# Kernel tuning notes

Hardware: AMD Instinct MI355X
Metric: run time of the kernel (lower is better)

Reference implementation:

```python
import jax, jax.numpy as jnp
import numpy as np

H = 4            # num_heads (forced: 128 projection / d_k=32)
DK = 32          # hardcoded d_k
SCALE = 1.0 / np.sqrt(32.0)
EPS = 1e-5       # LayerNorm eps (torch default)


def setup_inputs() -> dict:
    key = jax.random.key(0)
    ks = jax.random.split(key, 8)
    B, L, Dq, Dkv, M = 16, 4096, 512, 512, 512
    def w(k, shape, fan_in):
        return (jax.random.normal(k, shape, jnp.float32) / np.sqrt(fan_in)).astype(jnp.float32)
    return {
        "Q_in":  jax.random.normal(ks[0], (B, L, Dq),  jnp.float32),
        "KV_in": jax.random.normal(ks[1], (B, L, Dkv), jnp.float32),
        "Wq":  w(ks[2], (Dq, 128), Dq),   "bq":  jnp.zeros((128,), jnp.float32),
        "Wk":  w(ks[3], (Dkv, 128), Dkv), "bk":  jnp.zeros((128,), jnp.float32),
        "Wv":  w(ks[4], (Dkv, 128), Dkv), "bv":  jnp.zeros((128,), jnp.float32),
        "Wo":  w(ks[5], (128, M), 128),   "bo":  jnp.zeros((M,), jnp.float32),
        "Wqo": w(ks[6], (128, M), 128),   "bqo": jnp.zeros((M,), jnp.float32),
        "gamma": jnp.ones((M,), jnp.float32),
        "beta":  jnp.zeros((M,), jnp.float32),
    }


def reference(Q_in, KV_in, Wq, bq, Wk, bk, Wv, bv, Wo, bo, Wqo, bqo, gamma, beta):
    B, L, _ = Q_in.shape
    Qm = Q_in @ Wq + bq          # (B, L, 128)
    Km = KV_in @ Wk + bk         # (B, L, 128)
    Vm = KV_in @ Wv + bv         # (B, L, 128)

    def heads(X):
        # view(B, L, H, DK).permute(0, 2, 3, 1) -> (B, H, DK, L)
        return X.reshape(B, L, H, DK).transpose(0, 2, 3, 1)

    Qh, Kh, Vh = heads(Qm), heads(Km), heads(Vm)
    # matmul contracts over the SEQUENCE dim -> feature-feature scores (B,H,DK,DK)
    scores = jnp.einsum('bhdl,bhel->bhde', Qh, Kh) * SCALE
    attn = jax.nn.softmax(scores, axis=-1)          # dropout = identity (eval)
    out_h = jnp.einsum('bhde,bhel->bhdl', attn, Vh)  # (B, H, DK, L)
    out_h = out_h.transpose(0, 3, 1, 2).reshape(B, L, H * DK)  # (B, L, 128)

    out = out_h @ Wo + bo        # (B, L, M)
    Qm_ = Qm @ Wqo + bqo         # (B, L, M)
    x = Qm_ + out
    mu = jnp.mean(x, axis=-1, keepdims=True)
    var = jnp.var(x, axis=-1, keepdims=True)
    y = (x - mu) * jax.lax.rsqrt(var + EPS) * gamma + beta
    return (y, attn)
```

## Files before the change

kernel.cpp:

```cpp
#include <hip/hip_runtime.h>
#include <hip/hip_bf16.h>

typedef __bf16 bf16x8 __attribute__((ext_vector_type(8)));
typedef float  f32x4  __attribute__((ext_vector_type(4)));

#define SCALE_QK 0.17677669529663687f
#define LDSS 40

__device__ __forceinline__ float b2f(ushort u) {
    __hip_bfloat16 h; *reinterpret_cast<ushort*>(&h) = u; return __bfloat162float(h);
}
__device__ __forceinline__ ushort f2b(float f) {
    __hip_bfloat16 h = __float2bfloat16(f); return *reinterpret_cast<ushort*>(&h);
}

__global__ void k_prep(const float* __restrict__ Wq, const float* __restrict__ Wk,
                       const float* __restrict__ Wv, const float* __restrict__ Wqo,
                       const float* __restrict__ Wo,
                       ushort* __restrict__ WqThi, ushort* __restrict__ WqTlo,
                       ushort* __restrict__ WkThi, ushort* __restrict__ WkTlo,
                       ushort* __restrict__ WvT,  ushort* __restrict__ WqoT,
                       ushort* __restrict__ WoB) {
    int idx = blockIdx.x * 256 + threadIdx.x;
    int mat = idx >> 16, i = idx & 65535;
    if (mat == 0) {
        int n = i >> 9, k = i & 511;
        float w = Wq[k * 128 + n];
        ushort hi = f2b(w);
        WqThi[i] = hi; WqTlo[i] = f2b(w - b2f(hi));
    } else if (mat == 1) {
        int n = i >> 9, k = i & 511;
        float w = Wk[k * 128 + n];
        ushort hi = f2b(w);
        WkThi[i] = hi; WkTlo[i] = f2b(w - b2f(hi));
    } else if (mat == 2) {
        int n = i >> 9, k = i & 511;
        WvT[i] = f2b(Wv[k * 128 + n]);
    } else if (mat == 3) {
        int n = i >> 7, k = i & 127;
        WqoT[i] = f2b(Wqo[k * 512 + n]);
    } else if (mat == 4) {
        WoB[i] = f2b(Wo[i]);
    }
}

__global__ __launch_bounds__(256) void k_proj_split(
        const float* __restrict__ A, const ushort* __restrict__ BThi,
        const ushort* __restrict__ BTlo, const float* __restrict__ bias,
        float* __restrict__ outF, ushort* __restrict__ outB) {
    __shared__ __align__(16) ushort AsH[128 * LDSS], AsL[128 * LDSS];
    __shared__ __align__(16) ushort BsH[128 * LDSS], BsL[128 * LDSS];
    const int row0 = blockIdx.x * 128;
    const int tid  = threadIdx.x;
    const int wid  = tid >> 6, lane = tid & 63;
    const int wm = wid >> 1, wn = wid & 1;
    const int quad = lane >> 4, l16 = lane & 15;
    const int sr = tid >> 2;
    const int sc = (tid & 3) * 8;

    f32x4 acc[4][4] = {};

    for (int k0 = 0; k0 < 512; k0 += 32) {
        __syncthreads();
#pragma unroll
        for (int p = 0; p < 2; ++p) {
            int r = sr + p * 64;
            float4 a0 = *(const float4*)&A[(size_t)(row0 + r) * 512 + k0 + sc];
            float4 a1 = *(const float4*)&A[(size_t)(row0 + r) * 512 + k0 + sc + 4];
            float av[8] = {a0.x, a0.y, a0.z, a0.w, a1.x, a1.y, a1.z, a1.w};
            union { uint4 v; ushort u[8]; } H, L;
#pragma unroll
            for (int i = 0; i < 8; ++i) {
                ushort hi = f2b(av[i]);
                H.u[i] = hi;
                L.u[i] = f2b(av[i] - b2f(hi));
            }
            *(uint4*)&AsH[r * LDSS + sc] = H.v;
            *(uint4*)&AsL[r * LDSS + sc] = L.v;
            uint4 bh = *(const uint4*)&BThi[(size_t)r * 512 + k0 + sc];
            uint4 bl = *(const uint4*)&BTlo[(size_t)r * 512 + k0 + sc];
            *(uint4*)&BsH[r * LDSS + sc] = bh;
            *(uint4*)&BsL[r * LDSS + sc] = bl;
        }
        __syncthreads();
        bf16x8 aH[4], aL[4], bH[4], bL[4];
#pragma unroll
        for (int i = 0; i < 4; ++i) {
            int ro = (wm * 64 + i * 16 + l16) * LDSS + quad * 8;
            aH[i] = *reinterpret_cast<const bf16x8*>(&AsH[ro]);
            aL[i] = *reinterpret_cast<const bf16x8*>(&AsL[ro]);
        }
#pragma unroll
        for (int j = 0; j < 4; ++j) {
            int ro = (wn * 64 + j * 16 + l16) * LDSS + quad * 8;
            bH[j] = *reinterpret_cast<const bf16x8*>(&BsH[ro]);
            bL[j] = *reinterpret_cast<const bf16x8*>(&BsL[ro]);
        }
#pragma unroll
        for (int i = 0; i < 4; ++i)
#pragma unroll
            for (int j = 0; j < 4; ++j) {
                acc[i][j] = __builtin_amdgcn_mfma_f32_16x16x32_bf16(aL[i], bH[j], acc[i][j], 0, 0, 0);
                acc[i][j] = __builtin_amdgcn_mfma_f32_16x16x32_bf16(aH[i], bL[j], acc[i][j], 0, 0, 0);
                acc[i][j] = __builtin_amdgcn_mfma_f32_16x16x32_bf16(aH[i], bH[j], acc[i][j], 0, 0, 0);
            }
    }

#pragma unroll
    for (int i = 0; i < 4; ++i)
#pragma unroll
        for (int j = 0; j < 4; ++j) {
            int ncol = wn * 64 + j * 16 + l16;
            float bv = bias[ncol];
#pragma unroll
            for (int r = 0; r < 4; ++r) {
                int mrow = row0 + wm * 64 + i * 16 + quad * 4 + r;
                float v = acc[i][j][r] + bv;
                if (outF) outF[(size_t)mrow * 128 + ncol] = v;
                if (outB) outB[(size_t)mrow * 128 + ncol] = f2b(v);
            }
        }
}

__global__ __launch_bounds__(256) void k_proj_plain(
        const float* __restrict__ A, const ushort* __restrict__ BT,
        const float* __restrict__ bias, ushort* __restrict__ outB) {
    __shared__ __align__(16) ushort As[128 * LDSS];
    __shared__ __align__(16) ushort Bs[128 * LDSS];
    const int row0 = blockIdx.x * 128;
    const int tid  = threadIdx.x;
    const int wid  = tid >> 6, lane = tid & 63;
    const int wm = wid >> 1, wn = wid & 1;
    const int quad = lane >> 4, l16 = lane & 15;
    const int sr = tid >> 2;
    const int sc = (tid & 3) * 8;

    f32x4 acc[4][4] = {};

    for (int k0 = 0; k0 < 512; k0 += 32) {
        __syncthreads();
#pragma unroll
        for (int p = 0; p < 2; ++p) {
            int r = sr + p * 64;
            float4 a0 = *(const float4*)&A[(size_t)(row0 + r) * 512 + k0 + sc];
            float4 a1 = *(const float4*)&A[(size_t)(row0 + r) * 512 + k0 + sc + 4];
            float av[8] = {a0.x, a0.y, a0.z, a0.w, a1.x, a1.y, a1.z, a1.w};
            union { uint4 v; ushort u[8]; } H;
#pragma unroll
            for (int i = 0; i < 8; ++i) H.u[i] = f2b(av[i]);
            *(uint4*)&As[r * LDSS + sc] = H.v;
            *(uint4*)&Bs[r * LDSS + sc] = *(const uint4*)&BT[(size_t)r * 512 + k0 + sc];
        }
        __syncthreads();
        bf16x8 aF[4], bF[4];
#pragma unroll
        for (int i = 0; i < 4; ++i)
            aF[i] = *reinterpret_cast<const bf16x8*>(&As[(wm * 64 + i * 16 + l16) * LDSS + quad * 8]);
#pragma unroll
        for (int j = 0; j < 4; ++j)
            bF[j] = *reinterpret_cast<const bf16x8*>(&Bs[(wn * 64 + j * 16 + l16) * LDSS + quad * 8]);
#pragma unroll
        for (int i = 0; i < 4; ++i)
#pragma unroll
            for (int j = 0; j < 4; ++j)
                acc[i][j] = __builtin_amdgcn_mfma_f32_16x16x32_bf16(aF[i], bF[j], acc[i][j], 0, 0, 0);
    }

#pragma unroll
    for (int i = 0; i < 4; ++i)
#pragma unroll
        for (int j = 0; j < 4; ++j) {
            int ncol = wn * 64 + j * 16 + l16;
            float bv = bias[ncol];
#pragma unroll
            for (int r = 0; r < 4; ++r) {
                int mrow = row0 + wm * 64 + i * 16 + quad * 4 + r;
                outB[(size_t)mrow * 128 + ncol] = f2b(acc[i][j][r] + bv);
            }
        }
}

__global__ __launch_bounds__(256) void k_scores(
        const float* __restrict__ Qm, const float* __restrict__ Km,
        float* __restrict__ partial) {
    int b = blockIdx.x, sp = blockIdx.y;
    int t = threadIdx.x;
    int h = t >> 6, tl = t & 63;
    int d0 = (tl >> 3) * 4, e0 = (tl & 7) * 4;
    const float* Qb = Qm + ((size_t)b * 4096 + sp * 128) * 128 + h * 32 + d0;
    const float* Kb = Km + ((size_t)b * 4096 + sp * 128) * 128 + h * 32 + e0;
    float acc[4][4] = {};
#pragma unroll 4
    for (int l = 0; l < 128; ++l) {
        float4 q4 = *(const float4*)(Qb + (size_t)l * 128);
        float4 k4 = *(const float4*)(Kb + (size_t)l * 128);
        float q[4] = {q4.x, q4.y, q4.z, q4.w};
        float k[4] = {k4.x, k4.y, k4.z, k4.w};
#pragma unroll
        for (int i = 0; i < 4; ++i)
#pragma unroll
            for (int j = 0; j < 4; ++j) acc[i][j] += q[i] * k[j];
    }
    float* P = partial + ((size_t)(sp * 64 + b * 4 + h)) * 1024;
#pragma unroll
    for (int i = 0; i < 4; ++i)
#pragma unroll
        for (int j = 0; j < 4; ++j)
            P[(d0 + i) * 32 + e0 + j] = acc[i][j];
}

__global__ __launch_bounds__(1024) void k_softmax(
        const float* __restrict__ partial, float* __restrict__ attnOut) {
    int bh = blockIdx.x;
    int e = threadIdx.x;
    int d = threadIdx.y;
    float s = 0.f;
#pragma unroll
    for (int sp = 0; sp < 32; ++sp)
        s += partial[((size_t)(sp * 64 + bh)) * 1024 + d * 32 + e];
    s *= SCALE_QK;
    float m = s;
    for (int off = 16; off; off >>= 1) m = fmaxf(m, __shfl_xor(m, off, 32));
    float p = __expf(s - m);
    float sum = p;
    for (int off = 16; off; off >>= 1) sum += __shfl_xor(sum, off, 32);
    p /= sum;
    attnOut[(size_t)bh * 1024 + d * 32 + e] = p;
}

__global__ __launch_bounds__(256) void k_wc(
        const float* __restrict__ attnF, const ushort* __restrict__ WoB,
        ushort* __restrict__ WcT) {
    int b = blockIdx.x >> 2, h = blockIdx.x & 3;
    __shared__ float aS[32 * 32];
    __shared__ __align__(16) ushort wS[32 * 512];
    int t = threadIdx.x;
    for (int i = t; i < 1024; i += 256)
        aS[i] = attnF[((size_t)(b * 4 + h)) * 1024 + i];
    for (int i = t; i < 2048; i += 256) {
        int r = i >> 6, c = (i & 63) * 8;
        *(uint4*)&wS[r * 512 + c] = *(const uint4*)&WoB[(size_t)(h * 32 + r) * 512 + c];
    }
    __syncthreads();
    int e = t & 31;
    int mg = t >> 5;
    for (int mi = 0; mi < 64; ++mi) {
        int m = mg * 64 + mi;
        float acc = 0.f;
#pragma unroll
        for (int d = 0; d < 32; ++d)
            acc += aS[d * 32 + e] * b2f(wS[d * 512 + m]);
        WcT[((size_t)b * 512 + m) * 128 + h * 32 + e] = f2b(acc);
    }
}

__global__ __launch_bounds__(256) void k_out_gemm(
        const ushort* __restrict__ Vm, const ushort* __restrict__ Qm,
        const ushort* __restrict__ WcT, const ushort* __restrict__ WqoT,
        const float* __restrict__ bo, const float* __restrict__ bqo,
        float* __restrict__ X) {
    __shared__ __align__(16) ushort As[128 * LDSS];
    __shared__ __align__(16) ushort Bs[128 * LDSS];
    const int col0 = blockIdx.x * 128;
    const int row0 = blockIdx.y * 128;
    const int b = row0 >> 12;
    const ushort* WcTb = WcT + (size_t)b * 512 * 128;
    const int tid = threadIdx.x;
    const int wid = tid >> 6, lane = tid & 63;
    const int wm = wid >> 1, wn = wid & 1;
    const int quad = lane >> 4, l16 = lane & 15;
    const int sr = tid >> 2;
    const int sc = (tid & 3) * 8;

    f32x4 acc[4][4] = {};

    for (int k0 = 0; k0 < 256; k0 += 32) {
        const ushort* Asrc; const ushort* Bsrc; int kk;
        if (k0 < 128) { Asrc = Vm; Bsrc = WcTb; kk = k0; }
        else          { Asrc = Qm; Bsrc = WqoT; kk = k0 - 128; }
        __syncthreads();
#pragma unroll
        for (int p = 0; p < 2; ++p) {
            int r = sr + p * 64;
            uint4 va = *(const uint4*)&Asrc[(size_t)(row0 + r) * 128 + kk + sc];
            uint4 vb = *(const uint4*)&Bsrc[(size_t)(col0 + r) * 128 + kk + sc];
            *(uint4*)&As[r * LDSS + sc] = va;
            *(uint4*)&Bs[r * LDSS + sc] = vb;
        }
        __syncthreads();
        bf16x8 aF[4], bF[4];
#pragma unroll
        for (int i = 0; i < 4; ++i)
            aF[i] = *reinterpret_cast<const bf16x8*>(&As[(wm * 64 + i * 16 + l16) * LDSS + quad * 8]);
#pragma unroll
        for (int j = 0; j < 4; ++j)
            bF[j] = *reinterpret_cast<const bf16x8*>(&Bs[(wn * 64 + j * 16 + l16) * LDSS + quad * 8]);
#pragma unroll
        for (int i = 0; i < 4; ++i)
#pragma unroll
            for (int j = 0; j < 4; ++j)
                acc[i][j] = __builtin_amdgcn_mfma_f32_16x16x32_bf16(aF[i], bF[j], acc[i][j], 0, 0, 0);
    }

#pragma unroll
    for (int i = 0; i < 4; ++i)
#pragma unroll
        for (int j = 0; j < 4; ++j) {
            int ncol = col0 + wn * 64 + j * 16 + l16;
            float bv = bo[ncol] + bqo[ncol];
#pragma unroll
            for (int r = 0; r < 4; ++r) {
                int mrow = row0 + wm * 64 + i * 16 + quad * 4 + r;
                X[(size_t)mrow * 512 + ncol] = acc[i][j][r] + bv;
            }
        }
}

__global__ __launch_bounds__(256) void k_ln(
        float* __restrict__ Y, const float* __restrict__ gamma,
        const float* __restrict__ beta) {
    int row = blockIdx.x * 4 + (threadIdx.x >> 6);
    int lane = threadIdx.x & 63;
    size_t base = (size_t)row * 512 + lane * 8;
    float4 v0 = *(const float4*)&Y[base];
    float4 v1 = *(const float4*)&Y[base + 4];
    float x[8] = {v0.x, v0.y, v0.z, v0.w, v1.x, v1.y, v1.z, v1.w};
    float s = 0.f, ss = 0.f;
#pragma unroll
    for (int i = 0; i < 8; ++i) { s += x[i]; ss += x[i] * x[i]; }
    for (int off = 32; off; off >>= 1) {
        s  += __shfl_xor(s,  off, 64);
        ss += __shfl_xor(ss, off, 64);
    }
    float mu = s * (1.f / 512.f);
    float var = ss * (1.f / 512.f) - mu * mu;
    float rstd = rsqrtf(var + 1e-5f);
    float4 g0 = *(const float4*)&gamma[lane * 8];
    float4 g1 = *(const float4*)&gamma[lane * 8 + 4];
    float4 b0 = *(const float4*)&beta[lane * 8];
    float4 b1 = *(const float4*)&beta[lane * 8 + 4];
    float g[8] = {g0.x, g0.y, g0.z, g0.w, g1.x, g1.y, g1.z, g1.w};
    float bt[8] = {b0.x, b0.y, b0.z, b0.w, b1.x, b1.y, b1.z, b1.w};
    float4 o0, o1;
    float* o = (float*)&o0;
#pragma unroll
    for (int i = 0; i < 4; ++i) ((float*)&o0)[i] = (x[i] - mu) * rstd * g[i] + bt[i];
#pragma unroll
    for (int i = 0; i < 4; ++i) ((float*)&o1)[i] = (x[i + 4] - mu) * rstd * g[i + 4] + bt[i + 4];
    (void)o;
    *(float4*)&Y[base] = o0;
    *(float4*)&Y[base + 4] = o1;
}

extern "C" void kernel_launch(void* const* d_in, const int* in_sizes, int n_in,
                              void* d_out, int out_size, void* d_ws, size_t ws_size,
                              hipStream_t stream) {
    const float* Qin   = (const float*)d_in[0];
    const float* KVin  = (const float*)d_in[1];
    const float* Wq    = (const float*)d_in[2];
    const float* bq    = (const float*)d_in[3];
    const float* Wk    = (const float*)d_in[4];
    const float* bk    = (const float*)d_in[5];
    const float* Wv    = (const float*)d_in[6];
    const float* bv    = (const float*)d_in[7];
    const float* Wo    = (const float*)d_in[8];
    const float* bo    = (const float*)d_in[9];
    const float* Wqo   = (const float*)d_in[10];
    const float* bqo   = (const float*)d_in[11];
    const float* gamma = (const float*)d_in[12];
    const float* beta  = (const float*)d_in[13];
    float* out = (float*)d_out;
    float* attnOut = out + 33554432;

    char* ws = (char*)d_ws;
    ushort* WqThi = (ushort*)(ws);
    ushort* WqTlo = (ushort*)(ws + 131072);
    ushort* WkThi = (ushort*)(ws + 262144);
    ushort* WkTlo = (ushort*)(ws + 393216);
    ushort* WvT   = (ushort*)(ws + 524288);
    ushort* WqoT  = (ushort*)(ws + 655360);
    ushort* WoB   = (ushort*)(ws + 786432);
    float*  QmF   = (float*) (ws + 917504);
    float*  KmF   = (float*) (ws + 34471936);
    ushort* QmB   = (ushort*)(ws + 68026368);
    ushort* VmB   = (ushort*)(ws + 84803584);
    float*  part  = (float*) (ws + 101580800);
    ushort* WcT   = (ushort*)(ws + 109969408);

    k_prep<<<1280, 256, 0, stream>>>(Wq, Wk, Wv, Wqo, Wo,
                                     WqThi, WqTlo, WkThi, WkTlo, WvT, WqoT, WoB);
    k_proj_split<<<512, 256, 0, stream>>>(Qin,  WqThi, WqTlo, bq, QmF, QmB);
    k_proj_split<<<512, 256, 0, stream>>>(KVin, WkThi, WkTlo, bk, KmF, nullptr);
    k_proj_plain<<<512, 256, 0, stream>>>(KVin, WvT, bv, VmB);
    k_scores<<<dim3(16, 32), 256, 0, stream>>>(QmF, KmF, part);
    k_softmax<<<64, dim3(32, 32), 0, stream>>>(part, attnOut);
    k_wc<<<64, 256, 0, stream>>>(attnOut, WoB, WcT);
    k_out_gemm<<<dim3(4, 512), 256, 0, stream>>>(VmB, QmB, WcT, WqoT, bo, bqo, out);
    k_ln<<<16384, 256, 0, stream>>>(out, gamma, beta);
}
```

Before: 506.6 us.

## Fuse K/V projections, softmax with Wc, and output GEMM with LayerNorm

```diff
diff --git a/kernel.cpp b/kernel.cpp
--- a/kernel.cpp
+++ b/kernel.cpp
@@ -77,13 +77,11 @@
             }
             *(uint4*)&AsH[r * LDSS + sc] = H.v;
             *(uint4*)&AsL[r * LDSS + sc] = L.v;
-            uint4 bh = *(const uint4*)&BThi[(size_t)r * 512 + k0 + sc];
-            uint4 bl = *(const uint4*)&BTlo[(size_t)r * 512 + k0 + sc];
-            *(uint4*)&BsH[r * LDSS + sc] = bh;
-            *(uint4*)&BsL[r * LDSS + sc] = bl;
-        }
-        __syncthreads();
-        bf16x8 aH[4], aL[4], bH[4], bL[4];
+            *(uint4*)&BsH[r * LDSS + sc] = *(const uint4*)&BThi[(size_t)r * 512 + k0 + sc];
+            *(uint4*)&BsL[r * LDSS + sc] = *(const uint4*)&BTlo[(size_t)r * 512 + k0 + sc];
+        }
+        __syncthreads();
+        bf16x8 aH[4], aL[4];
 #pragma unroll
         for (int i = 0; i < 4; ++i) {
             int ro = (wm * 64 + i * 16 + l16) * LDSS + quad * 8;
@@ -93,17 +91,15 @@
 #pragma unroll
         for (int j = 0; j < 4; ++j) {
             int ro = (wn * 64 + j * 16 + l16) * LDSS + quad * 8;
-            bH[j] = *reinterpret_cast<const bf16x8*>(&BsH[ro]);
-            bL[j] = *reinterpret_cast<const bf16x8*>(&BsL[ro]);
-        }
-#pragma unroll
-        for (int i = 0; i < 4; ++i)
-#pragma unroll
-            for (int j = 0; j < 4; ++j) {
-                acc[i][j] = __builtin_amdgcn_mfma_f32_16x16x32_bf16(aL[i], bH[j], acc[i][j], 0, 0, 0);
-                acc[i][j] = __builtin_amdgcn_mfma_f32_16x16x32_bf16(aH[i], bL[j], acc[i][j], 0, 0, 0);
-                acc[i][j] = __builtin_amdgcn_mfma_f32_16x16x32_bf16(aH[i], bH[j], acc[i][j], 0, 0, 0);
-            }
+            bf16x8 bH = *reinterpret_cast<const bf16x8*>(&BsH[ro]);
+            bf16x8 bL = *reinterpret_cast<const bf16x8*>(&BsL[ro]);
+#pragma unroll
+            for (int i = 0; i < 4; ++i) {
+                acc[i][j] = __builtin_amdgcn_mfma_f32_16x16x32_bf16(aL[i], bH, acc[i][j], 0, 0, 0);
+                acc[i][j] = __builtin_amdgcn_mfma_f32_16x16x32_bf16(aH[i], bL, acc[i][j], 0, 0, 0);
+                acc[i][j] = __builtin_amdgcn_mfma_f32_16x16x32_bf16(aH[i], bH, acc[i][j], 0, 0, 0);
+            }
+        }
     }
 
 #pragma unroll
@@ -122,11 +118,14 @@
         }
 }
 
-__global__ __launch_bounds__(256) void k_proj_plain(
-        const float* __restrict__ A, const ushort* __restrict__ BT,
-        const float* __restrict__ bias, ushort* __restrict__ outB) {
-    __shared__ __align__(16) ushort As[128 * LDSS];
-    __shared__ __align__(16) ushort Bs[128 * LDSS];
+__global__ __launch_bounds__(256) void k_proj_kv(
+        const float* __restrict__ A,
+        const ushort* __restrict__ BKhi, const ushort* __restrict__ BKlo,
+        const ushort* __restrict__ BV,
+        const float* __restrict__ biasK, const float* __restrict__ biasV,
+        float* __restrict__ KmF, ushort* __restrict__ VmB) {
+    __shared__ __align__(16) ushort AsH[128 * LDSS], AsL[128 * LDSS];
+    __shared__ __align__(16) ushort BsKH[128 * LDSS], BsKL[128 * LDSS], BsV[128 * LDSS];
     const int row0 = blockIdx.x * 128;
     const int tid  = threadIdx.x;
     const int wid  = tid >> 6, lane = tid & 63;
@@ -135,7 +134,8 @@
     const int sr = tid >> 2;
     const int sc = (tid & 3) * 8;
 
-    f32x4 acc[4][4] = {};
+    f32x4 accK[4][4] = {};
+    f32x4 accV[4][4] = {};
 
     for (int k0 = 0; k0 < 512; k0 += 32) {
         __syncthreads();
@@ -145,25 +145,41 @@
             float4 a0 = *(const float4*)&A[(size_t)(row0 + r) * 512 + k0 + sc];
             float4 a1 = *(const float4*)&A[(size_t)(row0 + r) * 512 + k0 + sc + 4];
             float av[8] = {a0.x, a0.y, a0.z, a0.w, a1.x, a1.y, a1.z, a1.w};
-            union { uint4 v; ushort u[8]; } H;
-#pragma unroll
-            for (int i = 0; i < 8; ++i) H.u[i] = f2b(av[i]);
-            *(uint4*)&As[r * LDSS + sc] = H.v;
-            *(uint4*)&Bs[r * LDSS + sc] = *(const uint4*)&BT[(size_t)r * 512 + k0 + sc];
-        }
-        __syncthreads();
-        bf16x8 aF[4], bF[4];
-#pragma unroll
-        for (int i = 0; i < 4; ++i)
-            aF[i] = *reinterpret_cast<const bf16x8*>(&As[(wm * 64 + i * 16 + l16) * LDSS + quad * 8]);
-#pragma unroll
-        for (int j = 0; j < 4; ++j)
-            bF[j] = *reinterpret_cast<const bf16x8*>(&Bs[(wn * 64 + j * 16 + l16) * LDSS + quad * 8]);
-#pragma unroll
-        for (int i = 0; i < 4; ++i)
-#pragma unroll
-            for (int j = 0; j < 4; ++j)
-                acc[i][j] = __builtin_amdgcn_mfma_f32_16x16x32_bf16(aF[i], bF[j], acc[i][j], 0, 0, 0);
+            union { uint4 v; ushort u[8]; } H, L;
+#pragma unroll
+            for (int i = 0; i < 8; ++i) {
+                ushort hi = f2b(av[i]);
+                H.u[i] = hi;
+                L.u[i] = f2b(av[i] - b2f(hi));
+            }
+            *(uint4*)&AsH[r * LDSS + sc] = H.v;
+            *(uint4*)&AsL[r * LDSS + sc] = L.v;
+            *(uint4*)&BsKH[r * LDSS + sc] = *(const uint4*)&BKhi[(size_t)r * 512 + k0 + sc];
+            *(uint4*)&BsKL[r * LDSS + sc] = *(const uint4*)&BKlo[(size_t)r * 512 + k0 + sc];
+            *(uint4*)&BsV [r * LDSS + sc] = *(const uint4*)&BV  [(size_t)r * 512 + k0 + sc];
+        }
+        __syncthreads();
+        bf16x8 aH[4], aL[4];
+#pragma unroll
+        for (int i = 0; i < 4; ++i) {
+            int ro = (wm * 64 + i * 16 + l16) * LDSS + quad * 8;
+            aH[i] = *reinterpret_cast<const bf16x8*>(&AsH[ro]);
+            aL[i] = *reinterpret_cast<const bf16x8*>(&AsL[ro]);
+        }
+#pragma unroll
+        for (int j = 0; j < 4; ++j) {
+            int ro = (wn * 64 + j * 16 + l16) * LDSS + quad * 8;
+            bf16x8 bKH = *reinterpret_cast<const bf16x8*>(&BsKH[ro]);
+            bf16x8 bKL = *reinterpret_cast<const bf16x8*>(&BsKL[ro]);
+            bf16x8 bV  = *reinterpret_cast<const bf16x8*>(&BsV [ro]);
+#pragma unroll
+            for (int i = 0; i < 4; ++i) {
+                accK[i][j] = __builtin_amdgcn_mfma_f32_16x16x32_bf16(aL[i], bKH, accK[i][j], 0, 0, 0);
+                accK[i][j] = __builtin_amdgcn_mfma_f32_16x16x32_bf16(aH[i], bKL, accK[i][j], 0, 0, 0);
+                accK[i][j] = __builtin_amdgcn_mfma_f32_16x16x32_bf16(aH[i], bKH, accK[i][j], 0, 0, 0);
+                accV[i][j] = __builtin_amdgcn_mfma_f32_16x16x32_bf16(aH[i], bV,  accV[i][j], 0, 0, 0);
+            }
+        }
     }
 
 #pragma unroll
@@ -171,11 +187,12 @@
 #pragma unroll
         for (int j = 0; j < 4; ++j) {
             int ncol = wn * 64 + j * 16 + l16;
-            float bv = bias[ncol];
+            float bk = biasK[ncol], bv = biasV[ncol];
 #pragma unroll
             for (int r = 0; r < 4; ++r) {
                 int mrow = row0 + wm * 64 + i * 16 + quad * 4 + r;
-                outB[(size_t)mrow * 128 + ncol] = f2b(acc[i][j][r] + bv);
+                KmF[(size_t)mrow * 128 + ncol] = accK[i][j][r] + bk;
+                VmB[(size_t)mrow * 128 + ncol] = f2b(accV[i][j][r] + bv);
             }
         }
 }
@@ -209,41 +226,40 @@
             P[(d0 + i) * 32 + e0 + j] = acc[i][j];
 }
 
-__global__ __launch_bounds__(1024) void k_softmax(
-        const float* __restrict__ partial, float* __restrict__ attnOut) {
-    int bh = blockIdx.x;
-    int e = threadIdx.x;
-    int d = threadIdx.y;
-    float s = 0.f;
-#pragma unroll
-    for (int sp = 0; sp < 32; ++sp)
-        s += partial[((size_t)(sp * 64 + bh)) * 1024 + d * 32 + e];
-    s *= SCALE_QK;
-    float m = s;
-    for (int off = 16; off; off >>= 1) m = fmaxf(m, __shfl_xor(m, off, 32));
-    float p = __expf(s - m);
-    float sum = p;
-    for (int off = 16; off; off >>= 1) sum += __shfl_xor(sum, off, 32);
-    p /= sum;
-    attnOut[(size_t)bh * 1024 + d * 32 + e] = p;
-}
-
-__global__ __launch_bounds__(256) void k_wc(
-        const float* __restrict__ attnF, const ushort* __restrict__ WoB,
-        ushort* __restrict__ WcT) {
-    int b = blockIdx.x >> 2, h = blockIdx.x & 3;
-    __shared__ float aS[32 * 32];
+__global__ __launch_bounds__(256) void k_attn(
+        const float* __restrict__ partial, const ushort* __restrict__ WoB,
+        float* __restrict__ attnOut, ushort* __restrict__ WcT) {
+    int bh = blockIdx.x; int b = bh >> 2, h = bh & 3;
+    __shared__ float aS[1024];
     __shared__ __align__(16) ushort wS[32 * 512];
     int t = threadIdx.x;
-    for (int i = t; i < 1024; i += 256)
-        aS[i] = attnF[((size_t)(b * 4 + h)) * 1024 + i];
+    for (int i = t; i < 1024; i += 256) {
+        float s = 0.f;
+#pragma unroll
+        for (int sp = 0; sp < 32; ++sp)
+            s += partial[(size_t)(sp * 64 + bh) * 1024 + i];
+        aS[i] = s * SCALE_QK;
+    }
     for (int i = t; i < 2048; i += 256) {
         int r = i >> 6, c = (i & 63) * 8;
         *(uint4*)&wS[r * 512 + c] = *(const uint4*)&WoB[(size_t)(h * 32 + r) * 512 + c];
     }
     __syncthreads();
-    int e = t & 31;
-    int mg = t >> 5;
+    if (t < 32) {
+        float m = -1e30f;
+#pragma unroll
+        for (int e = 0; e < 32; ++e) m = fmaxf(m, aS[t * 32 + e]);
+        float p[32]; float sum = 0.f;
+#pragma unroll
+        for (int e = 0; e < 32; ++e) { p[e] = __expf(aS[t * 32 + e] - m); sum += p[e]; }
+        float inv = 1.f / sum;
+#pragma unroll
+        for (int e = 0; e < 32; ++e) aS[t * 32 + e] = p[e] * inv;
+    }
+    __syncthreads();
+    for (int i = t; i < 1024; i += 256)
+        attnOut[(size_t)bh * 1024 + i] = aS[i];
+    int e = t & 31, mg = t >> 5;
     for (int mi = 0; mi < 64; ++mi) {
         int m = mg * 64 + mi;
         float acc = 0.f;
@@ -254,102 +270,121 @@
     }
 }
 
-__global__ __launch_bounds__(256) void k_out_gemm(
+__global__ __launch_bounds__(256) void k_out_ln(
         const ushort* __restrict__ Vm, const ushort* __restrict__ Qm,
         const ushort* __restrict__ WcT, const ushort* __restrict__ WqoT,
         const float* __restrict__ bo, const float* __restrict__ bqo,
-        float* __restrict__ X) {
-    __shared__ __align__(16) ushort As[128 * LDSS];
-    __shared__ __align__(16) ushort Bs[128 * LDSS];
-    const int col0 = blockIdx.x * 128;
-    const int row0 = blockIdx.y * 128;
+        const float* __restrict__ gamma, const float* __restrict__ beta,
+        float* __restrict__ Y) {
+    __shared__ __align__(16) ushort As[64 * LDSS];
+    __shared__ __align__(16) ushort Bs[512 * LDSS];
+    __shared__ float sumS[4][64], sumSS[4][64], muA[64], rsA[64];
+    const int row0 = blockIdx.x * 64;
     const int b = row0 >> 12;
     const ushort* WcTb = WcT + (size_t)b * 512 * 128;
     const int tid = threadIdx.x;
     const int wid = tid >> 6, lane = tid & 63;
-    const int wm = wid >> 1, wn = wid & 1;
     const int quad = lane >> 4, l16 = lane & 15;
     const int sr = tid >> 2;
     const int sc = (tid & 3) * 8;
 
-    f32x4 acc[4][4] = {};
+    f32x4 acc[4][8] = {};
 
     for (int k0 = 0; k0 < 256; k0 += 32) {
         const ushort* Asrc; const ushort* Bsrc; int kk;
         if (k0 < 128) { Asrc = Vm; Bsrc = WcTb; kk = k0; }
         else          { Asrc = Qm; Bsrc = WqoT; kk = k0 - 128; }
         __syncthreads();
-#pragma unroll
-        for (int p = 0; p < 2; ++p) {
+        *(uint4*)&As[sr * LDSS + sc] =
+            *(const uint4*)&Asrc[(size_t)(row0 + sr) * 128 + kk + sc];
+#pragma unroll
+        for (int p = 0; p < 8; ++p) {
             int r = sr + p * 64;
-            uint4 va = *(const uint4*)&Asrc[(size_t)(row0 + r) * 128 + kk + sc];
-            uint4 vb = *(const uint4*)&Bsrc[(size_t)(col0 + r) * 128 + kk + sc];
-            *(uint4*)&As[r * LDSS + sc] = va;
-            *(uint4*)&Bs[r * LDSS + sc] = vb;
-        }
-        __syncthreads();
-        bf16x8 aF[4], bF[4];
+            *(uint4*)&Bs[r * LDSS + sc] = *(const uint4*)&Bsrc[(size_t)r * 128 + kk + sc];
+        }
+        __syncthreads();
+        bf16x8 aF[4];
 #pragma unroll
         for (int i = 0; i < 4; ++i)
-            aF[i] = *reinterpret_cast<const bf16x8*>(&As[(wm * 64 + i * 16 + l16) * LDSS + quad * 8]);
-#pragma unroll
-        for (int j = 0; j < 4; ++j)
-            bF[j] = *reinterpret_cast<const bf16x8*>(&Bs[(wn * 64 + j * 16 + l16) * LDSS + quad * 8]);
+            aF[i] = *reinterpret_cast<const bf16x8*>(&As[(i * 16 + l16) * LDSS + quad * 8]);
+#pragma unroll
+        for (int j = 0; j < 8; ++j) {
+            bf16x8 bF = *reinterpret_cast<const bf16x8*>(
+                &Bs[(wid * 128 + j * 16 + l16) * LDSS + quad * 8]);
+#pragma unroll
+            for (int i = 0; i < 4; ++i)
+                acc[i][j] = __builtin_amdgcn_mfma_f32_16x16x32_bf16(aF[i], bF, acc[i][j], 0, 0, 0);
+        }
+    }
+
+    float bv[8];
+#pragma unroll
+    for (int j = 0; j < 8; ++j) {
+        int ncol = wid * 128 + j * 16 + l16;
+        bv[j] = bo[ncol] + bqo[ncol];
+    }
+    float sArr[4][4], ssArr[4][4];
+#pragma unroll
+    for (int i = 0; i < 4; ++i)
+#pragma unroll
+        for (int r = 0; r < 4; ++r) {
+            float s = 0.f, ss = 0.f;
+#pragma unroll
+            for (int j = 0; j < 8; ++j) {
+                float x = acc[i][j][r] + bv[j];
+                s += x; ss += x * x;
+            }
+            sArr[i][r] = s; ssArr[i][r] = ss;
+        }
+#pragma unroll
+    for (int off = 1; off < 16; off <<= 1)
 #pragma unroll
         for (int i = 0; i < 4; ++i)
 #pragma unroll
-            for (int j = 0; j < 4; ++j)
-                acc[i][j] = __builtin_amdgcn_mfma_f32_16x16x32_bf16(aF[i], bF[j], acc[i][j], 0, 0, 0);
-    }
-
+            for (int r = 0; r < 4; ++r) {
+                sArr[i][r]  += __shfl_xor(sArr[i][r],  off, 64);
+                ssArr[i][r] += __shfl_xor(ssArr[i][r], off, 64);
+            }
+    if (l16 == 0) {
+#pragma unroll
+        for (int i = 0; i < 4; ++i)
+#pragma unroll
+            for (int r = 0; r < 4; ++r) {
+                int row = i * 16 + quad * 4 + r;
+                sumS[wid][row]  = sArr[i][r];
+                sumSS[wid][row] = ssArr[i][r];
+            }
+    }
+    __syncthreads();
+    if (tid < 64) {
+        float s = sumS[0][tid] + sumS[1][tid] + sumS[2][tid] + sumS[3][tid];
+        float ss = sumSS[0][tid] + sumSS[1][tid] + sumSS[2][tid] + sumSS[3][tid];
+        float mu = s * (1.f / 512.f);
+        float var = ss * (1.f / 512.f) - mu * mu;
+        muA[tid] = mu;
+        rsA[tid] = rsqrtf(var + 1e-5f);
+    }
+    __syncthreads();
+
+    float gj[8], bj[8];
+#pragma unroll
+    for (int j = 0; j < 8; ++j) {
+        int ncol = wid * 128 + j * 16 + l16;
+        gj[j] = gamma[ncol]; bj[j] = beta[ncol];
+    }
 #pragma unroll
     for (int i = 0; i < 4; ++i)
 #pragma unroll
-        for (int j = 0; j < 4; ++j) {
-            int ncol = col0 + wn * 64 + j * 16 + l16;
-            float bv = bo[ncol] + bqo[ncol];
-#pragma unroll
-            for (int r = 0; r < 4; ++r) {
-                int mrow = row0 + wm * 64 + i * 16 + quad * 4 + r;
-                X[(size_t)mrow * 512 + ncol] = acc[i][j][r] + bv;
-            }
-        }
-}
-
-__global__ __launch_bounds__(256) void k_ln(
-        float* __restrict__ Y, const float* __restrict__ gamma,
-        const float* __restrict__ beta) {
-    int row = blockIdx.x * 4 + (threadIdx.x >> 6);
-    int lane = threadIdx.x & 63;
-    size_t base = (size_t)row * 512 + lane * 8;
-    float4 v0 = *(const float4*)&Y[base];
-    float4 v1 = *(const float4*)&Y[base + 4];
-    float x[8] = {v0.x, v0.y, v0.z, v0.w, v1.x, v1.y, v1.z, v1.w};
-    float s = 0.f, ss = 0.f;
-#pragma unroll
-    for (int i = 0; i < 8; ++i) { s += x[i]; ss += x[i] * x[i]; }
-    for (int off = 32; off; off >>= 1) {
-        s  += __shfl_xor(s,  off, 64);
-        ss += __shfl_xor(ss, off, 64);
-    }
-    float mu = s * (1.f / 512.f);
-    float var = ss * (1.f / 512.f) - mu * mu;
-    float rstd = rsqrtf(var + 1e-5f);
-    float4 g0 = *(const float4*)&gamma[lane * 8];
-    float4 g1 = *(const float4*)&gamma[lane * 8 + 4];
-    float4 b0 = *(const float4*)&beta[lane * 8];
-    float4 b1 = *(const float4*)&beta[lane * 8 + 4];
-    float g[8] = {g0.x, g0.y, g0.z, g0.w, g1.x, g1.y, g1.z, g1.w};
-    float bt[8] = {b0.x, b0.y, b0.z, b0.w, b1.x, b1.y, b1.z, b1.w};
-    float4 o0, o1;
-    float* o = (float*)&o0;
-#pragma unroll
-    for (int i = 0; i < 4; ++i) ((float*)&o0)[i] = (x[i] - mu) * rstd * g[i] + bt[i];
-#pragma unroll
-    for (int i = 0; i < 4; ++i) ((float*)&o1)[i] = (x[i + 4] - mu) * rstd * g[i + 4] + bt[i + 4];
-    (void)o;
-    *(float4*)&Y[base] = o0;
-    *(float4*)&Y[base + 4] = o1;
+        for (int r = 0; r < 4; ++r) {
+            int row = i * 16 + quad * 4 + r;
+            float mu = muA[row], rstd = rsA[row];
+            size_t base = (size_t)(row0 + row) * 512 + wid * 128 + l16;
+#pragma unroll
+            for (int j = 0; j < 8; ++j) {
+                float x = acc[i][j][r] + bv[j];
+                Y[base + j * 16] = (x - mu) * rstd * gj[j] + bj[j];
+            }
+        }
 }
 
 extern "C" void kernel_launch(void* const* d_in, const int* in_sizes, int n_in,
@@ -389,12 +424,9 @@
 
     k_prep<<<1280, 256, 0, stream>>>(Wq, Wk, Wv, Wqo, Wo,
                                      WqThi, WqTlo, WkThi, WkTlo, WvT, WqoT, WoB);
-    k_proj_split<<<512, 256, 0, stream>>>(Qin,  WqThi, WqTlo, bq, QmF, QmB);
-    k_proj_split<<<512, 256, 0, stream>>>(KVin, WkThi, WkTlo, bk, KmF, nullptr);
-    k_proj_plain<<<512, 256, 0, stream>>>(KVin, WvT, bv, VmB);
+    k_proj_split<<<512, 256, 0, stream>>>(Qin, WqThi, WqTlo, bq, QmF, QmB);
+    k_proj_kv<<<512, 256, 0, stream>>>(KVin, WkThi, WkTlo, WvT, bk, bv, KmF, VmB);
     k_scores<<<dim3(16, 32), 256, 0, stream>>>(QmF, KmF, part);
-    k_softmax<<<64, dim3(32, 32), 0, stream>>>(part, attnOut);
-    k_wc<<<64, 256, 0, stream>>>(attnOut, WoB, WcT);
-    k_out_gemm<<<dim3(4, 512), 256, 0, stream>>>(VmB, QmB, WcT, WqoT, bo, bqo, out);
-    k_ln<<<16384, 256, 0, stream>>>(out, gamma, beta);
-}
+    k_attn<<<64, 256, 0, stream>>>(part, WoB, attnOut, WcT);
+    k_out_ln<<<1024, 256, 0, stream>>>(VmB, QmB, WcT, WqoT, bo, bqo, gamma, beta, out);
+}
```

Measured after the change: 485.9 us. -4.1%, faster.
